# Optimization experiments

Measured on AMD Instinct MI355X. Metric: run time of the kernel, lower is better.

The kernel has to match this reference:

```python
import jax, jax.numpy as jnp
import numpy as np

EMBED = 768
HEADS = 12


def setup_inputs() -> dict:
    key = jax.random.key(0)
    k1, k2, k3, k4, k5 = jax.random.split(key, 5)
    B, N, E = 8, 1024, EMBED
    x = jax.random.normal(k1, (B, N, E), dtype=jnp.float32)
    # torch Linear stored as [in, out] here (math-equivalent: y = x @ W + b)
    w_qkv = jax.random.normal(k2, (E, 3 * E), dtype=jnp.float32) * (E ** -0.5)
    b_qkv = jax.random.normal(k3, (3 * E,), dtype=jnp.float32) * 0.02
    w_proj = jax.random.normal(k4, (E, E), dtype=jnp.float32) * (E ** -0.5)
    b_proj = jax.random.normal(k5, (E,), dtype=jnp.float32) * 0.02
    return {"x": x, "w_qkv": w_qkv, "b_qkv": b_qkv, "w_proj": w_proj, "b_proj": b_proj}


def reference(x, w_qkv, b_qkv, w_proj, b_proj):
    B, N, E = x.shape
    H = HEADS
    D = E // H
    qkv = x @ w_qkv + b_qkv                       # [B, N, 3E]
    # rearrange 'b n (h d qkv) -> qkv b h n d': qkv index is innermost in last dim
    qkv = qkv.reshape(B, N, H, D, 3)
    qkv = jnp.transpose(qkv, (4, 0, 2, 1, 3))      # [3, B, H, N, D]
    q, k, v = qkv[0], qkv[1], qkv[2]
    energy = jnp.einsum('bhqd,bhkd->bhqk', q, k)   # [B, H, N, N]
    scaling = float(E) ** 0.5
    # NOTE: original scales AFTER softmax (unusual but faithful)
    att = jax.nn.softmax(energy, axis=-1) / scaling
    # dropout_prob = 0.0 -> identity
    out = jnp.einsum('bhqk,bhkd->bhqd', att, v)    # [B, H, N, D]
    out = jnp.transpose(out, (0, 2, 1, 3)).reshape(B, N, E)
    return out @ w_proj + b_proj
```

## Files before the change

kernel.cpp:

```cpp
#include <hip/hip_runtime.h>
#include <hip/hip_bf16.h>
#include <stdint.h>

#define NSEQ 1024
#define EMB 768
#define HEADS 12
#define HD 64
#define BATCH 8
#define BHN (BATCH*HEADS)

typedef __attribute__((ext_vector_type(8))) short bf16x8;
typedef __attribute__((ext_vector_type(4))) short bf16x4;
typedef __attribute__((ext_vector_type(4))) float f32x4;

typedef const void __attribute__((address_space(1))) cglobal_void;
typedef void __attribute__((address_space(3))) lds_void_t;

#define LOG2E 1.4426950408889634f

__device__ __forceinline__ void load_lds16(const void* g, void* l) {
    __builtin_amdgcn_global_load_lds((cglobal_void*)g, (lds_void_t*)l, 16, 0, 0);
}

__device__ __forceinline__ unsigned short f2bf(float f) {
    __hip_bfloat16 h = __float2bfloat16(f);
    return *reinterpret_cast<unsigned short*>(&h);
}

__device__ __forceinline__ unsigned int cvt_pk_bf16(float lo, float hi) {
    unsigned int r;
    asm("v_cvt_pk_bf16_f32 %0, %1, %2" : "=v"(r) : "v"(lo), "v"(hi));
    return r;
}

__device__ __forceinline__ float exp2_hw(float x) {
#if __has_builtin(__builtin_amdgcn_exp2f)
    return __builtin_amdgcn_exp2f(x);
#else
    return exp2f(x);
#endif
}

__global__ void conv_x_kernel(const float* __restrict__ x, unsigned short* __restrict__ xb) {
    int i = (blockIdx.x * 256 + threadIdx.x) * 4;
    float4 v = *reinterpret_cast<const float4*>(x + i);
    ushort4 o;
    o.x = f2bf(v.x); o.y = f2bf(v.y); o.z = f2bf(v.z); o.w = f2bf(v.w);
    *reinterpret_cast<ushort4*>(xb + i) = o;
}

template <int PERM>
__global__ void transpose_w_kernel(const float* __restrict__ w, unsigned short* __restrict__ wt,
                                   int K, int C) {
    __shared__ unsigned short tile[64][65];
    int c0 = blockIdx.x * 64;
    int k0 = blockIdx.y * 64;
    int t = threadIdx.x;
    int r = t >> 2, cc = (t & 3) * 16;
#pragma unroll
    for (int e = 0; e < 16; e += 4) {
        float4 v = *reinterpret_cast<const float4*>(w + (size_t)(k0 + r) * C + c0 + cc + e);
        float s0 = (PERM && ((c0 + cc + e + 0) % 3 == 0)) ? LOG2E : 1.0f;
        float s1 = (PERM && ((c0 + cc + e + 1) % 3 == 0)) ? LOG2E : 1.0f;
        float s2 = (PERM && ((c0 + cc + e + 2) % 3 == 0)) ? LOG2E : 1.0f;
        float s3 = (PERM && ((c0 + cc + e + 3) % 3 == 0)) ? LOG2E : 1.0f;
        tile[r][cc + e + 0] = f2bf(v.x * s0);
        tile[r][cc + e + 1] = f2bf(v.y * s1);
        tile[r][cc + e + 2] = f2bf(v.z * s2);
        tile[r][cc + e + 3] = f2bf(v.w * s3);
    }
    __syncthreads();
    int c = t >> 2, kk0 = (t & 3) * 16;
    int cg = c0 + c;
    int n;
    if (PERM) {
        int qkv = cg % 3, h = cg / 192, d = (cg % 192) / 3;
        n = qkv * EMB + h * HD + d;
    } else {
        n = cg;
    }
    uint4 lo, hi;
    lo.x = (unsigned)tile[kk0 + 0][c] | ((unsigned)tile[kk0 + 1][c] << 16);
    lo.y = (unsigned)tile[kk0 + 2][c] | ((unsigned)tile[kk0 + 3][c] << 16);
    lo.z = (unsigned)tile[kk0 + 4][c] | ((unsigned)tile[kk0 + 5][c] << 16);
    lo.w = (unsigned)tile[kk0 + 6][c] | ((unsigned)tile[kk0 + 7][c] << 16);
    hi.x = (unsigned)tile[kk0 + 8][c] | ((unsigned)tile[kk0 + 9][c] << 16);
    hi.y = (unsigned)tile[kk0 + 10][c] | ((unsigned)tile[kk0 + 11][c] << 16);
    hi.z = (unsigned)tile[kk0 + 12][c] | ((unsigned)tile[kk0 + 13][c] << 16);
    hi.w = (unsigned)tile[kk0 + 14][c] | ((unsigned)tile[kk0 + 15][c] << 16);
    *reinterpret_cast<uint4*>(wt + (size_t)n * K + k0 + kk0) = lo;
    *reinterpret_cast<uint4*>(wt + (size_t)n * K + k0 + kk0 + 8) = hi;
}

__global__ void perm_bias_kernel(const float* __restrict__ b, float* __restrict__ bp) {
    int c = blockIdx.x * 256 + threadIdx.x;
    int qkv = c % 3, h = c / 192, d = (c % 192) / 3;
    bp[qkv * EMB + h * HD + d] = (qkv == 0) ? b[c] * LOG2E : b[c];
}

__launch_bounds__(256, 4)
__global__ void gemm_qkv_kernel(const unsigned short* __restrict__ A,
                                const unsigned short* __restrict__ Bt,
                                const float* __restrict__ bias,
                                unsigned short* __restrict__ qout,
                                unsigned short* __restrict__ kout,
                                unsigned short* __restrict__ vout) {
    constexpr int TN = 18;
    constexpr int NWG = 64 * TN;
    constexpr int CHUNK = NWG / 8;
    constexpr int K = EMB;
    __shared__ unsigned short lds_a[128 * 64];
    __shared__ unsigned short lds_b[128 * 64];
    int bx0 = blockIdx.x;
    int bx = (bx0 % 8) * CHUNK + bx0 / 8;
    int tm = bx / TN, tn = bx % TN;
    bool vpath = (tn >= 12);
    const unsigned short* Bt_eff = Bt + (vpath ? (size_t)1536 * K : (size_t)0);
    const float* bias_eff = bias + (vpath ? 1536 : 0);
    int n0 = (vpath ? tn - 12 : tn) * 128;
    int m0 = tm * 128;
    int t = threadIdx.x;
    int l = t & 63;
    int g = l >> 4, c16 = l & 15;
    int wr = (t >> 7) & 1, wc = (t >> 6) & 1;
    int wbase = (t & 192);

    const char* baseA_f = vpath ? (const char*)lds_b : (const char*)lds_a;
    const char* baseB_f = vpath ? (const char*)lds_a : (const char*)lds_b;
    int roA = (vpath ? wc : wr) * 64;
    int roB = (vpath ? wr : wc) * 64;

    f32x4 acc[4][4];
#pragma unroll
    for (int i = 0; i < 4; i++)
#pragma unroll
        for (int j = 0; j < 4; j++)
#pragma unroll
            for (int r = 0; r < 4; r++) acc[i][j][r] = 0.f;

    for (int kt = 0; kt < K; kt += 64) {
        __syncthreads();
#pragma unroll
        for (int i = 0; i < 4; i++) {
            int c = i * 256 + t;
            int row = c >> 3;
            int sc = ((c & 7) ^ (row & 7)) * 8;
            load_lds16(A + (size_t)(m0 + row) * K + kt + sc, lds_a + (size_t)(i * 256 + wbase) * 8);
            load_lds16(Bt_eff + (size_t)(n0 + row) * K + kt + sc, lds_b + (size_t)(i * 256 + wbase) * 8);
        }
        __syncthreads();
#pragma unroll
        for (int kk = 0; kk < 2; kk++) {
            int cb = kk * 64 + g * 16;
            bf16x8 fa[4], fb[4];
#pragma unroll
            for (int i = 0; i < 4; i++) {
                int row = roA + i * 16 + c16;
                fa[i] = *reinterpret_cast<const bf16x8*>(
                    baseA_f + row * 128 + (cb ^ ((row & 7) << 4)));
            }
#pragma unroll
            for (int j = 0; j < 4; j++) {
                int row = roB + j * 16 + c16;
                fb[j] = *reinterpret_cast<const bf16x8*>(
                    baseB_f + row * 128 + (cb ^ ((row & 7) << 4)));
            }
#pragma unroll
            for (int i = 0; i < 4; i++)
#pragma unroll
                for (int j = 0; j < 4; j++)
                    acc[i][j] = __builtin_amdgcn_mfma_f32_16x16x32_bf16(fa[i], fb[j], acc[i][j], 0, 0, 0);
        }
    }

    if (vpath) {
#pragma unroll
        for (int i = 0; i < 4; i++) {
#pragma unroll
            for (int r = 0; r < 4; r++) {
                int nv = wc * 64 + i * 16 + (g * 4) + r + n0;
                float bv = bias_eff[nv];
                int hh = nv >> 6, dd = nv & 63;
#pragma unroll
                for (int j = 0; j < 4; j++) {
                    int m_g = m0 + wr * 64 + j * 16 + c16;
                    int bb = m_g >> 10, nn = m_g & 1023;
                    int nnp = (nn & ~31) | ((nn & 12) << 1) | ((nn >> 2) & 4) | (nn & 3);
                    vout[((size_t)(bb * HEADS + hh) * HD + dd) * NSEQ + nnp] =
                        f2bf(acc[i][j][r] + bv);
                }
            }
        }
    } else {
#pragma unroll
        for (int i = 0; i < 4; i++) {
            int mbase = m0 + wr * 64 + i * 16 + (g * 4);
#pragma unroll
            for (int j = 0; j < 4; j++) {
                int n_g = n0 + wc * 64 + j * 16 + c16;
                float bv = bias_eff[n_g];
#pragma unroll
                for (int r = 0; r < 4; r++) {
                    int m_g = mbase + r;
                    float v = acc[i][j][r] + bv;
                    int rem = n_g - ((n_g >= 768) ? 768 : 0);
                    int hh = rem >> 6, dd = rem & 63;
                    int bb = m_g >> 10, nn = m_g & 1023;
                    if (n_g < 768)
                        qout[(size_t)((bb * HEADS + hh) * NSEQ + nn) * HD + dd] = f2bf(v);
                    else
                        kout[(size_t)((bb * HEADS + hh) * NSEQ + nn) * HD + dd] = f2bf(v);
                }
            }
        }
    }
}

__launch_bounds__(256, 4)
__global__ void proj_kernel(const unsigned short* __restrict__ A,
                            const unsigned short* __restrict__ Bt,
                            const float* __restrict__ bias,
                            float* __restrict__ out) {
    constexpr int TN = 6;
    constexpr int NWG = 128 * TN;
    constexpr int CHUNK = NWG / 8;
    constexpr int K = EMB;
    __shared__ unsigned short lds_a[64 * 64];
    __shared__ unsigned short lds_b[128 * 64];
    int bx0 = blockIdx.x;
    int bx = (bx0 % 8) * CHUNK + bx0 / 8;
    int tm = bx / TN, tn = bx % TN;
    int m0 = tm * 64, n0 = tn * 128;
    int t = threadIdx.x;
    int l = t & 63;
    int g = l >> 4, c16 = l & 15;
    int w = t >> 6;
    int wbase = (t & 192);

    f32x4 acc[4][2];
#pragma unroll
    for (int i = 0; i < 4; i++)
#pragma unroll
        for (int j = 0; j < 2; j++)
#pragma unroll
            for (int r = 0; r < 4; r++) acc[i][j][r] = 0.f;

    for (int kt = 0; kt < K; kt += 64) {
        __syncthreads();
#pragma unroll
        for (int i = 0; i < 2; i++) {
            int c = i * 256 + t;
            int row = c >> 3;
            int sc = ((c & 7) ^ (row & 7)) * 8;
            load_lds16(A + (size_t)(m0 + row) * K + kt + sc, lds_a + (size_t)(i * 256 + wbase) * 8);
        }
#pragma unroll
        for (int i = 0; i < 4; i++) {
            int c = i * 256 + t;
            int row = c >> 3;
            int sc = ((c & 7) ^ (row & 7)) * 8;
            load_lds16(Bt + (size_t)(n0 + row) * K + kt + sc, lds_b + (size_t)(i * 256 + wbase) * 8);
        }
        __syncthreads();
#pragma unroll
        for (int kk = 0; kk < 2; kk++) {
            int cb = kk * 64 + g * 16;
            bf16x8 fa[4], fb[2];
#pragma unroll
            for (int i = 0; i < 4; i++) {
                int row = i * 16 + c16;
                fa[i] = *reinterpret_cast<const bf16x8*>(
                    (const char*)lds_a + row * 128 + (cb ^ ((row & 7) << 4)));
            }
#pragma unroll
            for (int j = 0; j < 2; j++) {
                int row = w * 32 + j * 16 + c16;
                fb[j] = *reinterpret_cast<const bf16x8*>(
                    (const char*)lds_b + row * 128 + (cb ^ ((row & 7) << 4)));
            }
#pragma unroll
            for (int i = 0; i < 4; i++)
#pragma unroll
                for (int j = 0; j < 2; j++)
                    acc[i][j] = __builtin_amdgcn_mfma_f32_16x16x32_bf16(fa[i], fb[j], acc[i][j], 0, 0, 0);
        }
    }

#pragma unroll
    for (int i = 0; i < 4; i++) {
        int mbase = m0 + i * 16 + g * 4;
#pragma unroll
        for (int j = 0; j < 2; j++) {
            int n_g = n0 + w * 32 + j * 16 + c16;
            float bv = bias[n_g];
#pragma unroll
            for (int r = 0; r < 4; r++)
                out[(size_t)(mbase + r) * EMB + n_g] = acc[i][j][r] + bv;
        }
    }
}

__launch_bounds__(256, 3)
__global__ void attn_kernel(const unsigned short* __restrict__ Q,
                            const unsigned short* __restrict__ K,
                            const unsigned short* __restrict__ Vt,
                            unsigned short* __restrict__ Oout) {
    __shared__ unsigned short k_lds[2][64 * 64];
    __shared__ unsigned short vt_lds[3][64 * 64];
    int bx = blockIdx.x;
    int bh = bx % BHN;
    int q0 = (bx / BHN) << 7;
    int b = bh / HEADS, h = bh % HEADS;
    int t = threadIdx.x, w = t >> 6, l = t & 63;
    int g = l >> 4, c16 = l & 15;
    const unsigned short* Qh = Q + (size_t)bh * NSEQ * HD;
    const unsigned short* Kh = K + (size_t)bh * NSEQ * HD;
    const unsigned short* Vth = Vt + (size_t)bh * NSEQ * HD;

    int qrA = q0 + w * 32 + c16;
    int qrB = qrA + 16;
    bf16x8 qfA[2], qfB[2];
    qfA[0] = *reinterpret_cast<const bf16x8*>(Qh + (size_t)qrA * HD + g * 8);
    qfA[1] = *reinterpret_cast<const bf16x8*>(Qh + (size_t)qrA * HD + 32 + g * 8);
    qfB[0] = *reinterpret_cast<const bf16x8*>(Qh + (size_t)qrB * HD + g * 8);
    qfB[1] = *reinterpret_cast<const bf16x8*>(Qh + (size_t)qrB * HD + 32 + g * 8);

    float lA = 0.f, lB = 0.f;
    f32x4 accA[4], accB[4];
#pragma unroll
    for (int jd = 0; jd < 4; jd++)
#pragma unroll
        for (int r = 0; r < 4; r++) { accA[jd][r] = 0.f; accB[jd][r] = 0.f; }

    auto stage = [&](unsigned short* kdst, unsigned short* vdst, int kv) {
#pragma unroll
        for (int i = 0; i < 2; i++) {
            int tt = i * 256 + t;
            int row = tt >> 3;
            int sc = ((tt & 7) ^ (row & 7)) * 8;
            load_lds16(Kh + (size_t)(kv + row) * HD + sc, kdst + (size_t)(tt & ~63) * 8);
            load_lds16(Vth + (size_t)row * NSEQ + kv + sc, vdst + (size_t)(tt & ~63) * 8);
        }
    };

    union PU { unsigned int u[4]; bf16x8 v; };
    bf16x8 pfA[2], pfB[2];
    auto softmax_pack = [&](f32x4 (&stA)[4], f32x4 (&stB)[4]) {
#pragma unroll
        for (int jk = 0; jk < 4; jk++)
#pragma unroll
            for (int r = 0; r < 4; r++) {
                stA[jk][r] = exp2_hw(stA[jk][r]);
                stB[jk][r] = exp2_hw(stB[jk][r]);
            }
        PU puA0, puA1, puB0, puB1;
#pragma unroll
        for (int p = 0; p < 2; p++) {
            puA0.u[p]     = cvt_pk_bf16(stA[0][2 * p], stA[0][2 * p + 1]);
            puA0.u[2 + p] = cvt_pk_bf16(stA[1][2 * p], stA[1][2 * p + 1]);
            puA1.u[p]     = cvt_pk_bf16(stA[2][2 * p], stA[2][2 * p + 1]);
            puA1.u[2 + p] = cvt_pk_bf16(stA[3][2 * p], stA[3][2 * p + 1]);
            puB0.u[p]     = cvt_pk_bf16(stB[0][2 * p], stB[0][2 * p + 1]);
            puB0.u[2 + p] = cvt_pk_bf16(stB[1][2 * p], stB[1][2 * p + 1]);
            puB1.u[p]     = cvt_pk_bf16(stB[2][2 * p], stB[2][2 * p + 1]);
            puB1.u[2 + p] = cvt_pk_bf16(stB[3][2 * p], stB[3][2 * p + 1]);
        }
        pfA[0] = puA0.v; pfA[1] = puA1.v;
        pfB[0] = puB0.v; pfB[1] = puB1.v;
        lA += (((stA[0][0] + stA[0][1]) + (stA[0][2] + stA[0][3])) +
               ((stA[1][0] + stA[1][1]) + (stA[1][2] + stA[1][3]))) +
              (((stA[2][0] + stA[2][1]) + (stA[2][2] + stA[2][3])) +
               ((stA[3][0] + stA[3][1]) + (stA[3][2] + stA[3][3])));
        lB += (((stB[0][0] + stB[0][1]) + (stB[0][2] + stB[0][3])) +
               ((stB[1][0] + stB[1][1]) + (stB[1][2] + stB[1][3]))) +
              (((stB[2][0] + stB[2][1]) + (stB[2][2] + stB[2][3])) +
               ((stB[3][0] + stB[3][1]) + (stB[3][2] + stB[3][3])));
    };

    auto qk_cluster = [&](const char* kbase, f32x4 (&stA)[4], f32x4 (&stB)[4]) {
#pragma unroll
        for (int kk = 0; kk < 2; kk++) {
            int cb = kk * 64 + g * 16;
#pragma unroll
            for (int jk = 0; jk < 4; jk++) {
                int row = jk * 16 + c16;
                bf16x8 kf = *reinterpret_cast<const bf16x8*>(
                    kbase + row * 128 + (cb ^ ((row & 7) << 4)));
                stA[jk] = __builtin_amdgcn_mfma_f32_16x16x32_bf16(kf, qfA[kk], stA[jk], 0, 0, 0);
                stB[jk] = __builtin_amdgcn_mfma_f32_16x16x32_bf16(kf, qfB[kk], stB[jk], 0, 0, 0);
            }
        }
    };
    auto pv_cluster = [&](const char* vbase) {
#pragma unroll
        for (int ks = 0; ks < 2; ks++) {
            int cb = ks * 64 + g * 16;
#pragma unroll
            for (int jd = 0; jd < 4; jd++) {
                int row = jd * 16 + c16;
                bf16x8 vf = *reinterpret_cast<const bf16x8*>(
                    vbase + row * 128 + (cb ^ ((row & 7) << 4)));
                accA[jd] = __builtin_amdgcn_mfma_f32_16x16x32_bf16(vf, pfA[ks], accA[jd], 0, 0, 0);
                accB[jd] = __builtin_amdgcn_mfma_f32_16x16x32_bf16(vf, pfB[ks], accB[jd], 0, 0, 0);
            }
        }
    };

    unsigned short* kcur = k_lds[0];
    unsigned short* knxt = k_lds[1];
    unsigned short* vprev = vt_lds[2];
    unsigned short* vcur  = vt_lds[0];
    unsigned short* vnxt  = vt_lds[1];

    stage(kcur, vcur, 0);
    __syncthreads();

    {
        stage(knxt, vnxt, 64);
        f32x4 stA[4], stB[4];
#pragma unroll
        for (int jk = 0; jk < 4; jk++)
#pragma unroll
            for (int r = 0; r < 4; r++) { stA[jk][r] = 0.f; stB[jk][r] = 0.f; }
        __builtin_amdgcn_s_setprio(1);
        qk_cluster((const char*)kcur, stA, stB);
        __builtin_amdgcn_s_setprio(0);
        softmax_pack(stA, stB);
        __syncthreads();
        unsigned short* tmp = kcur; kcur = knxt; knxt = tmp;
        unsigned short* tv = vprev; vprev = vcur; vcur = vnxt; vnxt = tv;
    }

#pragma unroll 1
    for (int it = 1; it < 16; ++it) {
        if (it < 15) stage(knxt, vnxt, (it + 1) << 6);
        f32x4 stA[4], stB[4];
#pragma unroll
        for (int jk = 0; jk < 4; jk++)
#pragma unroll
            for (int r = 0; r < 4; r++) { stA[jk][r] = 0.f; stB[jk][r] = 0.f; }
        __builtin_amdgcn_s_setprio(1);
        qk_cluster((const char*)kcur, stA, stB);
        pv_cluster((const char*)vprev);
        __builtin_amdgcn_s_setprio(0);
        softmax_pack(stA, stB);
        __syncthreads();
        unsigned short* tmp = kcur; kcur = knxt; knxt = tmp;
        unsigned short* tv = vprev; vprev = vcur; vcur = vnxt; vnxt = tv;
    }

    __builtin_amdgcn_s_setprio(1);
    pv_cluster((const char*)vprev);
    __builtin_amdgcn_s_setprio(0);

    lA += __shfl_xor(lA, 16);
    lA += __shfl_xor(lA, 32);
    lB += __shfl_xor(lB, 16);
    lB += __shfl_xor(lB, 32);
    const float scale = 27.712812921102035f;
    float invA = 1.0f / (lA * scale);
    float invB = 1.0f / (lB * scale);
    size_t qbaseA = ((size_t)(b * NSEQ + qrA) * HEADS + h) * HD;
    size_t qbaseB = ((size_t)(b * NSEQ + qrB) * HEADS + h) * HD;
#pragma unroll
    for (int jd = 0; jd < 4; jd++)
#pragma unroll
        for (int r = 0; r < 4; r++) {
            int d = jd * 16 + g * 4 + r;
            Oout[qbaseA + d] = f2bf(accA[jd][r] * invA);
            Oout[qbaseB + d] = f2bf(accB[jd][r] * invB);
        }
}

extern "C" void kernel_launch(void* const* d_in, const int* in_sizes, int n_in,
                              void* d_out, int out_size, void* d_ws, size_t ws_size,
                              hipStream_t stream) {
    const float* x = (const float*)d_in[0];
    const float* w_qkv = (const float*)d_in[1];
    const float* b_qkv = (const float*)d_in[2];
    const float* w_proj = (const float*)d_in[3];
    const float* b_proj = (const float*)d_in[4];

    char* ws = (char*)d_ws;
    unsigned short* xb      = (unsigned short*)(ws + 0);
    unsigned short* wt_qkv  = (unsigned short*)(ws + 12582912);
    unsigned short* wt_proj = (unsigned short*)(ws + 16121856);
    float*          biasp   = (float*)(ws + 17301504);
    unsigned short* qb      = (unsigned short*)(ws + 17310720);
    unsigned short* kb      = (unsigned short*)(ws + 29893632);
    unsigned short* vtb     = (unsigned short*)(ws + 42476544);
    unsigned short* ao      = (unsigned short*)(ws + 55059456);

    conv_x_kernel<<<6144, 256, 0, stream>>>(x, xb);
    transpose_w_kernel<1><<<dim3(36, 12), 256, 0, stream>>>(w_qkv, wt_qkv, EMB, 3 * EMB);
    transpose_w_kernel<0><<<dim3(12, 12), 256, 0, stream>>>(w_proj, wt_proj, EMB, EMB);
    perm_bias_kernel<<<9, 256, 0, stream>>>(b_qkv, biasp);

    gemm_qkv_kernel<<<64 * 18, 256, 0, stream>>>(xb, wt_qkv, biasp, qb, kb, vtb);
    attn_kernel<<<BHN * 8, 256, 0, stream>>>(qb, kb, vtb, ao);
    proj_kernel<<<128 * 6, 256, 0, stream>>>(ao, wt_proj, b_proj, (float*)d_out);
}
```

Baseline: 101.9 us.

## Replace QKV and projection GEMMs with a triple-buffered 256x128-tile GEMM template

Replaces the two separate GEMM kernels with one templated 512-thread kernel that uses 256x128 output tiles and a 3-stage LDS ring. Global-to-LDS loads for the next two K-steps are issued ahead, with vmcnt-based waits and raw s_barrier in place of the two __syncthreads per K-step, and s_setprio raised around the MFMA block. The aim is to hide global load latency and reuse each staged tile across more MFMAs. The QKV GEMM is split into two launches, one for Q/K and one for the transposed V path, so the 1536-wide and 768-wide parts no longer share a grid. The trade-off is fewer workgroups (384, 192 and 192) on a large GPU, which risks poor CU occupancy and wave-quantization tails, plus a large LDS footprint.

```diff
diff --git a/kernel.cpp b/kernel.cpp
--- a/kernel.cpp
+++ b/kernel.cpp
@@ -10,7 +10,6 @@
 #define BHN (BATCH*HEADS)
 
 typedef __attribute__((ext_vector_type(8))) short bf16x8;
-typedef __attribute__((ext_vector_type(4))) short bf16x4;
 typedef __attribute__((ext_vector_type(4))) float f32x4;
 
 typedef const void __attribute__((address_space(1))) cglobal_void;
@@ -98,204 +97,159 @@
     bp[qkv * EMB + h * HD + d] = (qkv == 0) ? b[c] * LOG2E : b[c];
 }
 
-__launch_bounds__(256, 4)
-__global__ void gemm_qkv_kernel(const unsigned short* __restrict__ A,
-                                const unsigned short* __restrict__ Bt,
-                                const float* __restrict__ bias,
-                                unsigned short* __restrict__ qout,
-                                unsigned short* __restrict__ kout,
-                                unsigned short* __restrict__ vout) {
-    constexpr int TN = 18;
-    constexpr int NWG = 64 * TN;
+template <int MODE>
+__launch_bounds__(512, 2)
+__global__ void gemm256_kernel(const unsigned short* __restrict__ A,
+                               const unsigned short* __restrict__ Bt,
+                               const float* __restrict__ bias,
+                               float* __restrict__ fout,
+                               unsigned short* __restrict__ uout,
+                               unsigned short* __restrict__ kout) {
+    constexpr int TN = (MODE == 0) ? 12 : 6;
+    constexpr int NWG = 32 * TN;
     constexpr int CHUNK = NWG / 8;
     constexpr int K = EMB;
-    __shared__ unsigned short lds_a[128 * 64];
-    __shared__ unsigned short lds_b[128 * 64];
+    constexpr int NT = K / 64;
+    __shared__ unsigned short lds[3][24576];
+
     int bx0 = blockIdx.x;
     int bx = (bx0 % 8) * CHUNK + bx0 / 8;
     int tm = bx / TN, tn = bx % TN;
-    bool vpath = (tn >= 12);
-    const unsigned short* Bt_eff = Bt + (vpath ? (size_t)1536 * K : (size_t)0);
-    const float* bias_eff = bias + (vpath ? 1536 : 0);
-    int n0 = (vpath ? tn - 12 : tn) * 128;
-    int m0 = tm * 128;
+    int m0 = tm * 256, n0 = tn * 128;
     int t = threadIdx.x;
     int l = t & 63;
     int g = l >> 4, c16 = l & 15;
-    int wr = (t >> 7) & 1, wc = (t >> 6) & 1;
-    int wbase = (t & 192);
-
-    const char* baseA_f = vpath ? (const char*)lds_b : (const char*)lds_a;
-    const char* baseB_f = vpath ? (const char*)lds_a : (const char*)lds_b;
-    int roA = (vpath ? wc : wr) * 64;
-    int roB = (vpath ? wr : wc) * 64;
-
-    f32x4 acc[4][4];
-#pragma unroll
-    for (int i = 0; i < 4; i++)
-#pragma unroll
-        for (int j = 0; j < 4; j++)
-#pragma unroll
-            for (int r = 0; r < 4; r++) acc[i][j][r] = 0.f;
-
-    for (int kt = 0; kt < K; kt += 64) {
-        __syncthreads();
-#pragma unroll
-        for (int i = 0; i < 4; i++) {
-            int c = i * 256 + t;
+    int wid = t >> 6;
+    int wm = wid >> 2, wn = wid & 3;
+    int wbase = t & ~63;
+
+    auto stage = [&](int buf, int kt) {
+        unsigned short* abase = lds[buf];
+#pragma unroll
+        for (int i4 = 0; i4 < 4; i4++) {
+            int c = i4 * 512 + t;
             int row = c >> 3;
             int sc = ((c & 7) ^ (row & 7)) * 8;
-            load_lds16(A + (size_t)(m0 + row) * K + kt + sc, lds_a + (size_t)(i * 256 + wbase) * 8);
-            load_lds16(Bt_eff + (size_t)(n0 + row) * K + kt + sc, lds_b + (size_t)(i * 256 + wbase) * 8);
-        }
-        __syncthreads();
+            load_lds16(A + (size_t)(m0 + row) * K + kt + sc,
+                       abase + (size_t)(i4 * 512 + wbase) * 8);
+        }
+        unsigned short* bbase = lds[buf] + 16384;
+#pragma unroll
+        for (int i2 = 0; i2 < 2; i2++) {
+            int c = i2 * 512 + t;
+            int row = c >> 3;
+            int sc = ((c & 7) ^ (row & 7)) * 8;
+            load_lds16(Bt + (size_t)(n0 + row) * K + kt + sc,
+                       bbase + (size_t)(i2 * 512 + wbase) * 8);
+        }
+    };
+
+    f32x4 acc[8][2];
+#pragma unroll
+    for (int q = 0; q < 8; q++)
+#pragma unroll
+        for (int p = 0; p < 2; p++)
+#pragma unroll
+            for (int r = 0; r < 4; r++) acc[q][p][r] = 0.f;
+
+    stage(0, 0);
+    stage(1, 64);
+
+#pragma unroll
+    for (int i = 0; i < NT; ++i) {
+        if (i + 2 < NT) {
+            stage((i + 2) % 3, (i + 2) * 64);
+            asm volatile("s_waitcnt vmcnt(12)\n\ts_barrier" ::: "memory");
+        } else if (i + 2 == NT) {
+            asm volatile("s_waitcnt vmcnt(6)\n\ts_barrier" ::: "memory");
+        } else {
+            asm volatile("s_waitcnt vmcnt(0)\n\ts_barrier" ::: "memory");
+        }
+        const char* bufA = (const char*)lds[i % 3];
+        const char* bufB = bufA + 32768;
+        __builtin_amdgcn_s_setprio(1);
 #pragma unroll
         for (int kk = 0; kk < 2; kk++) {
             int cb = kk * 64 + g * 16;
-            bf16x8 fa[4], fb[4];
-#pragma unroll
-            for (int i = 0; i < 4; i++) {
-                int row = roA + i * 16 + c16;
-                fa[i] = *reinterpret_cast<const bf16x8*>(
-                    baseA_f + row * 128 + (cb ^ ((row & 7) << 4)));
-            }
-#pragma unroll
-            for (int j = 0; j < 4; j++) {
-                int row = roB + j * 16 + c16;
-                fb[j] = *reinterpret_cast<const bf16x8*>(
-                    baseB_f + row * 128 + (cb ^ ((row & 7) << 4)));
-            }
-#pragma unroll
-            for (int i = 0; i < 4; i++)
-#pragma unroll
-                for (int j = 0; j < 4; j++)
-                    acc[i][j] = __builtin_amdgcn_mfma_f32_16x16x32_bf16(fa[i], fb[j], acc[i][j], 0, 0, 0);
-        }
-    }
-
-    if (vpath) {
-#pragma unroll
-        for (int i = 0; i < 4; i++) {
+            bf16x8 fa[8], fb[2];
+#pragma unroll
+            for (int q = 0; q < 8; q++) {
+                int row = wm * 128 + q * 16 + c16;
+                fa[q] = *reinterpret_cast<const bf16x8*>(
+                    bufA + row * 128 + (cb ^ ((row & 7) << 4)));
+            }
+#pragma unroll
+            for (int p = 0; p < 2; p++) {
+                int row = wn * 32 + p * 16 + c16;
+                fb[p] = *reinterpret_cast<const bf16x8*>(
+                    bufB + row * 128 + (cb ^ ((row & 7) << 4)));
+            }
+#pragma unroll
+            for (int q = 0; q < 8; q++)
+#pragma unroll
+                for (int p = 0; p < 2; p++) {
+                    if (MODE == 1)
+                        acc[q][p] = __builtin_amdgcn_mfma_f32_16x16x32_bf16(fb[p], fa[q], acc[q][p], 0, 0, 0);
+                    else
+                        acc[q][p] = __builtin_amdgcn_mfma_f32_16x16x32_bf16(fa[q], fb[p], acc[q][p], 0, 0, 0);
+                }
+        }
+        __builtin_amdgcn_s_setprio(0);
+        asm volatile("s_barrier" ::: "memory");
+    }
+
+    if (MODE == 0) {
+#pragma unroll
+        for (int q = 0; q < 8; q++) {
+            int mbase = m0 + wm * 128 + q * 16 + g * 4;
+#pragma unroll
+            for (int p = 0; p < 2; p++) {
+                int n_g = n0 + wn * 32 + p * 16 + c16;
+                float bv = bias[n_g];
+                int rem = n_g - ((n_g >= 768) ? 768 : 0);
+                int hh = rem >> 6, dd = rem & 63;
+#pragma unroll
+                for (int r = 0; r < 4; r++) {
+                    int m_g = mbase + r;
+                    int bb = m_g >> 10, nn = m_g & 1023;
+                    unsigned short val = f2bf(acc[q][p][r] + bv);
+                    if (n_g < 768)
+                        uout[(size_t)((bb * HEADS + hh) * NSEQ + nn) * HD + dd] = val;
+                    else
+                        kout[(size_t)((bb * HEADS + hh) * NSEQ + nn) * HD + dd] = val;
+                }
+            }
+        }
+    } else if (MODE == 1) {
+#pragma unroll
+        for (int p = 0; p < 2; p++) {
 #pragma unroll
             for (int r = 0; r < 4; r++) {
-                int nv = wc * 64 + i * 16 + (g * 4) + r + n0;
-                float bv = bias_eff[nv];
+                int nv = n0 + wn * 32 + p * 16 + g * 4 + r;
+                float bv = bias[nv];
                 int hh = nv >> 6, dd = nv & 63;
 #pragma unroll
-                for (int j = 0; j < 4; j++) {
-                    int m_g = m0 + wr * 64 + j * 16 + c16;
+                for (int q = 0; q < 8; q++) {
+                    int m_g = m0 + wm * 128 + q * 16 + c16;
                     int bb = m_g >> 10, nn = m_g & 1023;
                     int nnp = (nn & ~31) | ((nn & 12) << 1) | ((nn >> 2) & 4) | (nn & 3);
-                    vout[((size_t)(bb * HEADS + hh) * HD + dd) * NSEQ + nnp] =
-                        f2bf(acc[i][j][r] + bv);
+                    uout[((size_t)(bb * HEADS + hh) * HD + dd) * NSEQ + nnp] =
+                        f2bf(acc[q][p][r] + bv);
                 }
             }
         }
     } else {
 #pragma unroll
-        for (int i = 0; i < 4; i++) {
-            int mbase = m0 + wr * 64 + i * 16 + (g * 4);
-#pragma unroll
-            for (int j = 0; j < 4; j++) {
-                int n_g = n0 + wc * 64 + j * 16 + c16;
-                float bv = bias_eff[n_g];
-#pragma unroll
-                for (int r = 0; r < 4; r++) {
-                    int m_g = mbase + r;
-                    float v = acc[i][j][r] + bv;
-                    int rem = n_g - ((n_g >= 768) ? 768 : 0);
-                    int hh = rem >> 6, dd = rem & 63;
-                    int bb = m_g >> 10, nn = m_g & 1023;
-                    if (n_g < 768)
-                        qout[(size_t)((bb * HEADS + hh) * NSEQ + nn) * HD + dd] = f2bf(v);
-                    else
-                        kout[(size_t)((bb * HEADS + hh) * NSEQ + nn) * HD + dd] = f2bf(v);
-                }
-            }
-        }
-    }
-}
-
-__launch_bounds__(256, 4)
-__global__ void proj_kernel(const unsigned short* __restrict__ A,
-                            const unsigned short* __restrict__ Bt,
-                            const float* __restrict__ bias,
-                            float* __restrict__ out) {
-    constexpr int TN = 6;
-    constexpr int NWG = 128 * TN;
-    constexpr int CHUNK = NWG / 8;
-    constexpr int K = EMB;
-    __shared__ unsigned short lds_a[64 * 64];
-    __shared__ unsigned short lds_b[128 * 64];
-    int bx0 = blockIdx.x;
-    int bx = (bx0 % 8) * CHUNK + bx0 / 8;
-    int tm = bx / TN, tn = bx % TN;
-    int m0 = tm * 64, n0 = tn * 128;
-    int t = threadIdx.x;
-    int l = t & 63;
-    int g = l >> 4, c16 = l & 15;
-    int w = t >> 6;
-    int wbase = (t & 192);
-
-    f32x4 acc[4][2];
-#pragma unroll
-    for (int i = 0; i < 4; i++)
-#pragma unroll
-        for (int j = 0; j < 2; j++)
-#pragma unroll
-            for (int r = 0; r < 4; r++) acc[i][j][r] = 0.f;
-
-    for (int kt = 0; kt < K; kt += 64) {
-        __syncthreads();
-#pragma unroll
-        for (int i = 0; i < 2; i++) {
-            int c = i * 256 + t;
-            int row = c >> 3;
-            int sc = ((c & 7) ^ (row & 7)) * 8;
-            load_lds16(A + (size_t)(m0 + row) * K + kt + sc, lds_a + (size_t)(i * 256 + wbase) * 8);
-        }
-#pragma unroll
-        for (int i = 0; i < 4; i++) {
-            int c = i * 256 + t;
-            int row = c >> 3;
-            int sc = ((c & 7) ^ (row & 7)) * 8;
-            load_lds16(Bt + (size_t)(n0 + row) * K + kt + sc, lds_b + (size_t)(i * 256 + wbase) * 8);
-        }
-        __syncthreads();
-#pragma unroll
-        for (int kk = 0; kk < 2; kk++) {
-            int cb = kk * 64 + g * 16;
-            bf16x8 fa[4], fb[2];
-#pragma unroll
-            for (int i = 0; i < 4; i++) {
-                int row = i * 16 + c16;
-                fa[i] = *reinterpret_cast<const bf16x8*>(
-                    (const char*)lds_a + row * 128 + (cb ^ ((row & 7) << 4)));
-            }
-#pragma unroll
-            for (int j = 0; j < 2; j++) {
-                int row = w * 32 + j * 16 + c16;
-                fb[j] = *reinterpret_cast<const bf16x8*>(
-                    (const char*)lds_b + row * 128 + (cb ^ ((row & 7) << 4)));
-            }
-#pragma unroll
-            for (int i = 0; i < 4; i++)
-#pragma unroll
-                for (int j = 0; j < 2; j++)
-                    acc[i][j] = __builtin_amdgcn_mfma_f32_16x16x32_bf16(fa[i], fb[j], acc[i][j], 0, 0, 0);
-        }
-    }
-
-#pragma unroll
-    for (int i = 0; i < 4; i++) {
-        int mbase = m0 + i * 16 + g * 4;
-#pragma unroll
-        for (int j = 0; j < 2; j++) {
-            int n_g = n0 + w * 32 + j * 16 + c16;
-            float bv = bias[n_g];
-#pragma unroll
-            for (int r = 0; r < 4; r++)
-                out[(size_t)(mbase + r) * EMB + n_g] = acc[i][j][r] + bv;
+        for (int q = 0; q < 8; q++) {
+            int mbase = m0 + wm * 128 + q * 16 + g * 4;
+#pragma unroll
+            for (int p = 0; p < 2; p++) {
+                int n_g = n0 + wn * 32 + p * 16 + c16;
+                float bv = bias[n_g];
+#pragma unroll
+                for (int r = 0; r < 4; r++)
+                    fout[(size_t)(mbase + r) * EMB + n_g] = acc[q][p][r] + bv;
+            }
         }
     }
 }
@@ -496,7 +450,10 @@
     transpose_w_kernel<0><<<dim3(12, 12), 256, 0, stream>>>(w_proj, wt_proj, EMB, EMB);
     perm_bias_kernel<<<9, 256, 0, stream>>>(b_qkv, biasp);
 
-    gemm_qkv_kernel<<<64 * 18, 256, 0, stream>>>(xb, wt_qkv, biasp, qb, kb, vtb);
+    gemm256_kernel<0><<<384, 512, 0, stream>>>(xb, wt_qkv, biasp, nullptr, qb, kb);
+    gemm256_kernel<1><<<192, 512, 0, stream>>>(xb, wt_qkv + (size_t)1536 * EMB, biasp + 1536,
+                                               nullptr, vtb, nullptr);
     attn_kernel<<<BHN * 8, 256, 0, stream>>>(qb, kb, vtb, ao);
-    proj_kernel<<<128 * 6, 256, 0, stream>>>(ao, wt_proj, b_proj, (float*)d_out);
-}
+    gemm256_kernel<2><<<192, 512, 0, stream>>>(ao, wt_proj, b_proj, (float*)d_out,
+                                               nullptr, nullptr);
+}
```

New measurement: 108.2 us. 6.2% more time.

## Software-pipeline attention softmax across iterations and merge prep kernels into one launch

Applied to the files above, without the earlier changes.

The attention main loop is unrolled by two with double-buffered score registers, so the softmax and pack for the previous tile run between the current QK MFMA cluster and the PV cluster. This lets exp and convert work overlap with matrix work. The row-sum accumulation is vectorised and reduced once at the end. The four preprocessing kernels (x conversion, the two weight transposes, bias permute) are merged into a single launch to cut launch overhead, at the cost of higher register pressure from holding two score sets.

```diff
diff --git a/kernel.cpp b/kernel.cpp
--- a/kernel.cpp
+++ b/kernel.cpp
@@ -10,7 +10,6 @@
 #define BHN (BATCH*HEADS)
 
 typedef __attribute__((ext_vector_type(8))) short bf16x8;
-typedef __attribute__((ext_vector_type(4))) short bf16x4;
 typedef __attribute__((ext_vector_type(4))) float f32x4;
 
 typedef const void __attribute__((address_space(1))) cglobal_void;
@@ -41,61 +40,72 @@
 #endif
 }
 
-__global__ void conv_x_kernel(const float* __restrict__ x, unsigned short* __restrict__ xb) {
-    int i = (blockIdx.x * 256 + threadIdx.x) * 4;
-    float4 v = *reinterpret_cast<const float4*>(x + i);
-    ushort4 o;
-    o.x = f2bf(v.x); o.y = f2bf(v.y); o.z = f2bf(v.z); o.w = f2bf(v.w);
-    *reinterpret_cast<ushort4*>(xb + i) = o;
-}
-
-template <int PERM>
-__global__ void transpose_w_kernel(const float* __restrict__ w, unsigned short* __restrict__ wt,
-                                   int K, int C) {
+__global__ void prep_kernel(const float* __restrict__ x, unsigned short* __restrict__ xb,
+                            const float* __restrict__ w_qkv, unsigned short* __restrict__ wt_qkv,
+                            const float* __restrict__ w_proj, unsigned short* __restrict__ wt_proj,
+                            const float* __restrict__ b_qkv, float* __restrict__ biasp) {
     __shared__ unsigned short tile[64][65];
-    int c0 = blockIdx.x * 64;
-    int k0 = blockIdx.y * 64;
-    int t = threadIdx.x;
-    int r = t >> 2, cc = (t & 3) * 16;
-#pragma unroll
-    for (int e = 0; e < 16; e += 4) {
-        float4 v = *reinterpret_cast<const float4*>(w + (size_t)(k0 + r) * C + c0 + cc + e);
-        float s0 = (PERM && ((c0 + cc + e + 0) % 3 == 0)) ? LOG2E : 1.0f;
-        float s1 = (PERM && ((c0 + cc + e + 1) % 3 == 0)) ? LOG2E : 1.0f;
-        float s2 = (PERM && ((c0 + cc + e + 2) % 3 == 0)) ? LOG2E : 1.0f;
-        float s3 = (PERM && ((c0 + cc + e + 3) % 3 == 0)) ? LOG2E : 1.0f;
-        tile[r][cc + e + 0] = f2bf(v.x * s0);
-        tile[r][cc + e + 1] = f2bf(v.y * s1);
-        tile[r][cc + e + 2] = f2bf(v.z * s2);
-        tile[r][cc + e + 3] = f2bf(v.w * s3);
-    }
-    __syncthreads();
-    int c = t >> 2, kk0 = (t & 3) * 16;
-    int cg = c0 + c;
-    int n;
-    if (PERM) {
-        int qkv = cg % 3, h = cg / 192, d = (cg % 192) / 3;
-        n = qkv * EMB + h * HD + d;
-    } else {
-        n = cg;
-    }
-    uint4 lo, hi;
-    lo.x = (unsigned)tile[kk0 + 0][c] | ((unsigned)tile[kk0 + 1][c] << 16);
-    lo.y = (unsigned)tile[kk0 + 2][c] | ((unsigned)tile[kk0 + 3][c] << 16);
-    lo.z = (unsigned)tile[kk0 + 4][c] | ((unsigned)tile[kk0 + 5][c] << 16);
-    lo.w = (unsigned)tile[kk0 + 6][c] | ((unsigned)tile[kk0 + 7][c] << 16);
-    hi.x = (unsigned)tile[kk0 + 8][c] | ((unsigned)tile[kk0 + 9][c] << 16);
-    hi.y = (unsigned)tile[kk0 + 10][c] | ((unsigned)tile[kk0 + 11][c] << 16);
-    hi.z = (unsigned)tile[kk0 + 12][c] | ((unsigned)tile[kk0 + 13][c] << 16);
-    hi.w = (unsigned)tile[kk0 + 14][c] | ((unsigned)tile[kk0 + 15][c] << 16);
-    *reinterpret_cast<uint4*>(wt + (size_t)n * K + k0 + kk0) = lo;
-    *reinterpret_cast<uint4*>(wt + (size_t)n * K + k0 + kk0 + 8) = hi;
-}
-
-__global__ void perm_bias_kernel(const float* __restrict__ b, float* __restrict__ bp) {
-    int c = blockIdx.x * 256 + threadIdx.x;
-    int qkv = c % 3, h = c / 192, d = (c % 192) / 3;
-    bp[qkv * EMB + h * HD + d] = (qkv == 0) ? b[c] * LOG2E : b[c];
+    int bx = blockIdx.x, t = threadIdx.x;
+    if (bx < 6144) {
+        int i = (bx * 256 + t) * 4;
+        float4 v = *reinterpret_cast<const float4*>(x + i);
+        ushort4 o;
+        o.x = f2bf(v.x); o.y = f2bf(v.y); o.z = f2bf(v.z); o.w = f2bf(v.w);
+        *reinterpret_cast<ushort4*>(xb + i) = o;
+        return;
+    }
+    if (bx < 6720) {
+        bool perm = (bx < 6576);
+        int bb = perm ? bx - 6144 : bx - 6576;
+        int tilesC = perm ? 36 : 12;
+        int C = perm ? 3 * EMB : EMB;
+        const float* w = perm ? w_qkv : w_proj;
+        unsigned short* wt = perm ? wt_qkv : wt_proj;
+        int c0 = (bb % tilesC) * 64, k0 = (bb / tilesC) * 64;
+        int r = t >> 2, cc = (t & 3) * 16;
+#pragma unroll
+        for (int e = 0; e < 16; e += 4) {
+            float4 v = *reinterpret_cast<const float4*>(w + (size_t)(k0 + r) * C + c0 + cc + e);
+            float s0 = (perm && ((c0 + cc + e + 0) % 3 == 0)) ? LOG2E : 1.0f;
+            float s1 = (perm && ((c0 + cc + e + 1) % 3 == 0)) ? LOG2E : 1.0f;
+            float s2 = (perm && ((c0 + cc + e + 2) % 3 == 0)) ? LOG2E : 1.0f;
+            float s3 = (perm && ((c0 + cc + e + 3) % 3 == 0)) ? LOG2E : 1.0f;
+            tile[r][cc + e + 0] = f2bf(v.x * s0);
+            tile[r][cc + e + 1] = f2bf(v.y * s1);
+            tile[r][cc + e + 2] = f2bf(v.z * s2);
+            tile[r][cc + e + 3] = f2bf(v.w * s3);
+        }
+        __syncthreads();
+        int c = t >> 2, kk0 = (t & 3) * 16;
+        int cg = c0 + c;
+        int n;
+        if (perm) {
+            int qkv = cg % 3, h = cg / 192, d = (cg % 192) / 3;
+            n = qkv * EMB + h * HD + d;
+        } else {
+            n = cg;
+        }
+        uint4 lo, hi;
+        lo.x = (unsigned)tile[kk0 + 0][c] | ((unsigned)tile[kk0 + 1][c] << 16);
+        lo.y = (unsigned)tile[kk0 + 2][c] | ((unsigned)tile[kk0 + 3][c] << 16);
+        lo.z = (unsigned)tile[kk0 + 4][c] | ((unsigned)tile[kk0 + 5][c] << 16);
+        lo.w = (unsigned)tile[kk0 + 6][c] | ((unsigned)tile[kk0 + 7][c] << 16);
+        hi.x = (unsigned)tile[kk0 + 8][c] | ((unsigned)tile[kk0 + 9][c] << 16);
+        hi.y = (unsigned)tile[kk0 + 10][c] | ((unsigned)tile[kk0 + 11][c] << 16);
+        hi.z = (unsigned)tile[kk0 + 12][c] | ((unsigned)tile[kk0 + 13][c] << 16);
+        hi.w = (unsigned)tile[kk0 + 14][c] | ((unsigned)tile[kk0 + 15][c] << 16);
+        *reinterpret_cast<uint4*>(wt + (size_t)n * EMB + k0 + kk0) = lo;
+        *reinterpret_cast<uint4*>(wt + (size_t)n * EMB + k0 + kk0 + 8) = hi;
+        return;
+    }
+    {
+        int c = (bx - 6720) * 256 + t;
+        if (c < 3 * EMB) {
+            int qkv = c % 3, h = c / 192, d = (c % 192) / 3;
+            biasp[qkv * EMB + h * HD + d] = (qkv == 0) ? b_qkv[c] * LOG2E : b_qkv[c];
+        }
+        return;
+    }
 }
 
 __launch_bounds__(256, 4)
@@ -325,7 +335,9 @@
     qfB[0] = *reinterpret_cast<const bf16x8*>(Qh + (size_t)qrB * HD + g * 8);
     qfB[1] = *reinterpret_cast<const bf16x8*>(Qh + (size_t)qrB * HD + 32 + g * 8);
 
-    float lA = 0.f, lB = 0.f;
+    f32x4 lAv, lBv;
+#pragma unroll
+    for (int r = 0; r < 4; r++) { lAv[r] = 0.f; lBv[r] = 0.f; }
     f32x4 accA[4], accB[4];
 #pragma unroll
     for (int jd = 0; jd < 4; jd++)
@@ -367,14 +379,8 @@
         }
         pfA[0] = puA0.v; pfA[1] = puA1.v;
         pfB[0] = puB0.v; pfB[1] = puB1.v;
-        lA += (((stA[0][0] + stA[0][1]) + (stA[0][2] + stA[0][3])) +
-               ((stA[1][0] + stA[1][1]) + (stA[1][2] + stA[1][3]))) +
-              (((stA[2][0] + stA[2][1]) + (stA[2][2] + stA[2][3])) +
-               ((stA[3][0] + stA[3][1]) + (stA[3][2] + stA[3][3])));
-        lB += (((stB[0][0] + stB[0][1]) + (stB[0][2] + stB[0][3])) +
-               ((stB[1][0] + stB[1][1]) + (stB[1][2] + stB[1][3]))) +
-              (((stB[2][0] + stB[2][1]) + (stB[2][2] + stB[2][3])) +
-               ((stB[3][0] + stB[3][1]) + (stB[3][2] + stB[3][3])));
+        lAv += (stA[0] + stA[1]) + (stA[2] + stA[3]);
+        lBv += (stB[0] + stB[1]) + (stB[2] + stB[3]);
     };
 
     auto qk_cluster = [&](const char* kbase, f32x4 (&stA)[4], f32x4 (&stB)[4]) {
@@ -406,53 +412,93 @@
         }
     };
 
+    f32x4 sA0[4], sB0[4], sA1[4], sB1[4];
+
     unsigned short* kcur = k_lds[0];
     unsigned short* knxt = k_lds[1];
     unsigned short* vprev = vt_lds[2];
     unsigned short* vcur  = vt_lds[0];
     unsigned short* vnxt  = vt_lds[1];
 
+    auto rotate = [&]() {
+        unsigned short* tmp = kcur; kcur = knxt; knxt = tmp;
+        unsigned short* tv = vprev; vprev = vcur; vcur = vnxt; vnxt = tv;
+    };
+
     stage(kcur, vcur, 0);
     __syncthreads();
 
     {
         stage(knxt, vnxt, 64);
-        f32x4 stA[4], stB[4];
 #pragma unroll
         for (int jk = 0; jk < 4; jk++)
 #pragma unroll
-            for (int r = 0; r < 4; r++) { stA[jk][r] = 0.f; stB[jk][r] = 0.f; }
+            for (int r = 0; r < 4; r++) { sA0[jk][r] = 0.f; sB0[jk][r] = 0.f; }
         __builtin_amdgcn_s_setprio(1);
-        qk_cluster((const char*)kcur, stA, stB);
+        qk_cluster((const char*)kcur, sA0, sB0);
         __builtin_amdgcn_s_setprio(0);
-        softmax_pack(stA, stB);
-        __syncthreads();
-        unsigned short* tmp = kcur; kcur = knxt; knxt = tmp;
-        unsigned short* tv = vprev; vprev = vcur; vcur = vnxt; vnxt = tv;
+        __syncthreads();
+        rotate();
     }
 
 #pragma unroll 1
-    for (int it = 1; it < 16; ++it) {
-        if (it < 15) stage(knxt, vnxt, (it + 1) << 6);
-        f32x4 stA[4], stB[4];
+    for (int tt = 1; tt < 15; tt += 2) {
+        {
+            stage(knxt, vnxt, (tt + 1) << 6);
+#pragma unroll
+            for (int jk = 0; jk < 4; jk++)
+#pragma unroll
+                for (int r = 0; r < 4; r++) { sA1[jk][r] = 0.f; sB1[jk][r] = 0.f; }
+            __builtin_amdgcn_s_setprio(1);
+            qk_cluster((const char*)kcur, sA1, sB1);
+            __builtin_amdgcn_s_setprio(0);
+            softmax_pack(sA0, sB0);
+            __builtin_amdgcn_s_setprio(1);
+            pv_cluster((const char*)vprev);
+            __builtin_amdgcn_s_setprio(0);
+            __syncthreads();
+            rotate();
+        }
+        {
+            stage(knxt, vnxt, (tt + 2) << 6);
+#pragma unroll
+            for (int jk = 0; jk < 4; jk++)
+#pragma unroll
+                for (int r = 0; r < 4; r++) { sA0[jk][r] = 0.f; sB0[jk][r] = 0.f; }
+            __builtin_amdgcn_s_setprio(1);
+            qk_cluster((const char*)kcur, sA0, sB0);
+            __builtin_amdgcn_s_setprio(0);
+            softmax_pack(sA1, sB1);
+            __builtin_amdgcn_s_setprio(1);
+            pv_cluster((const char*)vprev);
+            __builtin_amdgcn_s_setprio(0);
+            __syncthreads();
+            rotate();
+        }
+    }
+
+    {
 #pragma unroll
         for (int jk = 0; jk < 4; jk++)
 #pragma unroll
-            for (int r = 0; r < 4; r++) { stA[jk][r] = 0.f; stB[jk][r] = 0.f; }
+            for (int r = 0; r < 4; r++) { sA1[jk][r] = 0.f; sB1[jk][r] = 0.f; }
         __builtin_amdgcn_s_setprio(1);
-        qk_cluster((const char*)kcur, stA, stB);
+        qk_cluster((const char*)kcur, sA1, sB1);
+        __builtin_amdgcn_s_setprio(0);
+        softmax_pack(sA0, sB0);
+        __builtin_amdgcn_s_setprio(1);
         pv_cluster((const char*)vprev);
         __builtin_amdgcn_s_setprio(0);
-        softmax_pack(stA, stB);
-        __syncthreads();
-        unsigned short* tmp = kcur; kcur = knxt; knxt = tmp;
-        unsigned short* tv = vprev; vprev = vcur; vcur = vnxt; vnxt = tv;
-    }
-
+        __syncthreads();
+        rotate();
+    }
+    softmax_pack(sA1, sB1);
     __builtin_amdgcn_s_setprio(1);
     pv_cluster((const char*)vprev);
     __builtin_amdgcn_s_setprio(0);
 
+    float lA = (lAv[0] + lAv[1]) + (lAv[2] + lAv[3]);
+    float lB = (lBv[0] + lBv[1]) + (lBv[2] + lBv[3]);
     lA += __shfl_xor(lA, 16);
     lA += __shfl_xor(lA, 32);
     lB += __shfl_xor(lB, 16);
@@ -491,10 +537,7 @@
     unsigned short* vtb     = (unsigned short*)(ws + 42476544);
     unsigned short* ao      = (unsigned short*)(ws + 55059456);
 
-    conv_x_kernel<<<6144, 256, 0, stream>>>(x, xb);
-    transpose_w_kernel<1><<<dim3(36, 12), 256, 0, stream>>>(w_qkv, wt_qkv, EMB, 3 * EMB);
-    transpose_w_kernel<0><<<dim3(12, 12), 256, 0, stream>>>(w_proj, wt_proj, EMB, EMB);
-    perm_bias_kernel<<<9, 256, 0, stream>>>(b_qkv, biasp);
+    prep_kernel<<<6729, 256, 0, stream>>>(x, xb, w_qkv, wt_qkv, w_proj, wt_proj, b_qkv, biasp);
 
     gemm_qkv_kernel<<<64 * 18, 256, 0, stream>>>(xb, wt_qkv, biasp, qb, kb, vtb);
     attn_kernel<<<BHN * 8, 256, 0, stream>>>(qb, kb, vtb, ao);
```

Result: no change. 101.3 us (-0.5%).
